# Kernel tuning notes

Measured on AMD Instinct MI355X. Metric: run time of the kernel, lower is better.

## Reference

```python
import jax, jax.numpy as jnp
import numpy as np

D_MODEL = 1024
N_HEADS = 16
D_HEAD = D_MODEL // N_HEADS
SCALE = float(np.sqrt(D_HEAD))


def setup_inputs() -> dict:
    key = jax.random.key(0)
    ks = jax.random.split(key, 9)
    B, S = 2, 2048
    x = jax.random.normal(ks[0], (B, S, D_MODEL), dtype=jnp.float32)
    mask = jnp.tril(jnp.ones((S, S), dtype=jnp.int32))  # causal mask, 0 = masked
    std = 1.0 / np.sqrt(D_MODEL)
    Wq = jax.random.normal(ks[1], (D_MODEL, D_MODEL), dtype=jnp.float32) * std
    bq = jnp.zeros((D_MODEL,), dtype=jnp.float32)
    Wk = jax.random.normal(ks[2], (D_MODEL, D_MODEL), dtype=jnp.float32) * std
    bk = jnp.zeros((D_MODEL,), dtype=jnp.float32)
    Wv = jax.random.normal(ks[3], (D_MODEL, D_MODEL), dtype=jnp.float32) * std
    bv = jnp.zeros((D_MODEL,), dtype=jnp.float32)
    Wo = jax.random.normal(ks[4], (D_MODEL, D_MODEL), dtype=jnp.float32) * std
    bo = jnp.zeros((D_MODEL,), dtype=jnp.float32)
    return {"x": x, "mask": mask, "Wq": Wq, "bq": bq, "Wk": Wk, "bk": bk,
            "Wv": Wv, "bv": bv, "Wo": Wo, "bo": bo}


def reference(x, mask, Wq, bq, Wk, bk, Wv, bv, Wo, bo):
    B, S, _ = x.shape
    # projections (PyTorch Linear: x @ W.T + b; here W stored as [in, out])
    Q = (x @ Wq + bq).reshape(B, S, N_HEADS, D_HEAD).transpose(0, 2, 1, 3)
    K = (x @ Wk + bk).reshape(B, S, N_HEADS, D_HEAD).transpose(0, 2, 1, 3)
    V = (x @ Wv + bv).reshape(B, S, N_HEADS, D_HEAD).transpose(0, 2, 1, 3)
    scores = jnp.einsum('bhqd,bhkd->bhqk', Q, K) / SCALE  # [B,H,S,S]
    scores = jnp.where(mask == 0, -jnp.inf, scores)
    attn = jax.nn.softmax(scores, axis=-1)  # dropout p=0 -> identity
    ctx = jnp.einsum('bhqk,bhkd->bhqd', attn, V)
    ctx = ctx.transpose(0, 2, 1, 3).reshape(B, S, D_MODEL)
    return ctx @ Wo + bo
```

## Files before the change

kernel.cpp:

```cpp
#include <hip/hip_runtime.h>
#include <stdint.h>
#include <math.h>

typedef unsigned short u16;
typedef __attribute__((ext_vector_type(8))) short short8;
typedef __attribute__((ext_vector_type(4))) float f32x4;

#define DEV __device__ __forceinline__

DEV u16 f2b(float f) {
  union { float f; uint32_t u; } v; v.f = f;
  uint32_t r = v.u + 0x7FFFu + ((v.u >> 16) & 1u);
  return (u16)(r >> 16);
}

DEV f32x4 mfma16(short8 a, short8 b, f32x4 c) {
  return __builtin_amdgcn_mfma_f32_16x16x32_bf16(a, b, c, 0, 0, 0);
}

DEV void gload_lds16(const void* g, void* l) {
  __builtin_amdgcn_global_load_lds(
      (const __attribute__((address_space(1))) void*)g,
      (__attribute__((address_space(3))) void*)l, 16, 0, 0);
}

__global__ __launch_bounds__(256) void pack_x_kernel(const float* __restrict__ x,
                                                     u16* __restrict__ xb) {
  int i = blockIdx.x * 256 + threadIdx.x;
  float4 v = reinterpret_cast<const float4*>(x)[i];
  ushort4 o;
  o.x = f2b(v.x); o.y = f2b(v.y); o.z = f2b(v.z); o.w = f2b(v.w);
  reinterpret_cast<ushort4*>(xb)[i] = o;
}

__global__ __launch_bounds__(256) void pack_w4_kernel(
    const float* __restrict__ W0, const float* __restrict__ W1,
    const float* __restrict__ W2, const float* __restrict__ W3,
    u16* __restrict__ T0, u16* __restrict__ T1, u16* __restrict__ T2, u16* __restrict__ T3) {
  const float* W; u16* T;
  switch (blockIdx.z) {
    case 0: W = W0; T = T0; break;
    case 1: W = W1; T = T1; break;
    case 2: W = W2; T = T2; break;
    default: W = W3; T = T3; break;
  }
  __shared__ float t[32][33];
  const int tx = threadIdx.x, ty = threadIdx.y;
  const int n0 = blockIdx.x * 32, k0 = blockIdx.y * 32;
#pragma unroll
  for (int i = 0; i < 32; i += 8)
    t[ty + i][tx] = W[(size_t)(k0 + ty + i) * 1024 + n0 + tx];
  __syncthreads();
#pragma unroll
  for (int i = 0; i < 32; i += 8)
    T[(size_t)(n0 + ty + i) * 1024 + k0 + tx] = f2b(t[tx][ty + i]);
}

template <int MODE>
__global__ __launch_bounds__(256) void gemm_bt_kernel(
    const u16* __restrict__ A, const u16* __restrict__ Bt,
    const float* __restrict__ bias, const float* __restrict__ bias2,
    void* __restrict__ out, int M_, int N_, int K_, float scale) {
  const int tid = threadIdx.x;
  const int w = tid >> 6, l = tid & 63;
  const int g = l >> 4, lr = l & 15;
  const int wr = w >> 1, wc = w & 1;
  const int bm = blockIdx.y, bn = blockIdx.x;

  __shared__ __align__(16) u16 Als[2][128 * 32];
  __shared__ __align__(16) u16 Bls[2][128 * 32];

  f32x4 acc[4][4] = {};

  const int nk = K_ >> 5;
  const int arow = tid >> 2;
  const int acol = (tid & 3) * 8;

  auto stage = [&](int buf, int kt) {
    const int kk = kt * 32 + acol;
#pragma unroll
    for (int i = 0; i < 2; ++i) {
      const u16* asrc = A + (size_t)(bm * 128 + i * 64 + arow) * K_ + kk;
      gload_lds16(asrc, (char*)&Als[buf][0] + i * 4096 + w * 1024);
      const u16* bsrc = Bt + (size_t)(bn * 128 + i * 64 + arow) * K_ + kk;
      gload_lds16(bsrc, (char*)&Bls[buf][0] + i * 4096 + w * 1024);
    }
  };

  stage(0, 0);
  __syncthreads();

  for (int kt = 0; kt < nk; ++kt) {
    const int cur = kt & 1;
    if (kt + 1 < nk) stage(cur ^ 1, kt + 1);
    short8 af[4], bf[4];
#pragma unroll
    for (int i = 0; i < 4; ++i)
      af[i] = *reinterpret_cast<const short8*>(&Als[cur][(wr * 64 + i * 16 + lr) * 32 + g * 8]);
#pragma unroll
    for (int j = 0; j < 4; ++j)
      bf[j] = *reinterpret_cast<const short8*>(&Bls[cur][(wc * 64 + j * 16 + lr) * 32 + g * 8]);
#pragma unroll
    for (int i = 0; i < 4; ++i)
#pragma unroll
      for (int j = 0; j < 4; ++j)
        acc[i][j] = mfma16(af[i], bf[j], acc[i][j]);
    __syncthreads();
  }

#pragma unroll
  for (int i = 0; i < 4; ++i) {
#pragma unroll
    for (int j = 0; j < 4; ++j) {
#pragma unroll
      for (int r = 0; r < 4; ++r) {
        const int row = bm * 128 + wr * 64 + i * 16 + g * 4 + r;
        const int col = bn * 128 + wc * 64 + j * 16 + lr;
        const float v = acc[i][j][r];
        if constexpr (MODE == 0) {
          ((float*)out)[(size_t)row * N_ + col] = v + bias[col];
        } else if constexpr (MODE == 2) {
          const int proj = col >> 10;
          const int c = col & 1023;
          const int b = row >> 11, s = row & 2047;
          const int h = c >> 6, d = c & 63;
          const float bi = proj ? bias2[c] : bias[c];
          const float sc = proj ? 1.0f : scale;
          ((u16*)out)[(size_t)proj * 4194304 +
                      (((size_t)(b * 16 + h)) * 2048 + s) * 64 + d] = f2b((v + bi) * sc);
        } else {
          const int b = col >> 11, s = col & 2047;
          ((u16*)out)[((size_t)(b * 1024 + row)) * 2048 + s] = f2b(v + bias[row]);
        }
      }
    }
  }
}

__global__ __launch_bounds__(256) void attn_kernel(
    const u16* __restrict__ Qg, const u16* __restrict__ Kg,
    const u16* __restrict__ Vt, u16* __restrict__ Og) {
  const int lin = blockIdx.x;
  const int xcd = lin & 7, jj = lin >> 3;
  const int bh = xcd * 4 + (jj >> 4);
  const int pair = jj & 15;
  const int b = bh >> 4, h = bh & 15;
  const int tid = threadIdx.x;
  const int w = tid >> 6, l = tid & 63;
  const int g = l >> 4, lr = l & 15;

  __shared__ __align__(16) u16 Kls[2][64 * 64];
  __shared__ __align__(16) u16 Vls[2][64 * 64];
  __shared__ __align__(16) u16 Pl[4][16 * 88];
  u16* myP = &Pl[w][0];

  const u16* Kbh = Kg + (size_t)bh * 2048 * 64;
  const u16* Vbh = Vt + ((size_t)(b * 1024 + h * 64)) * 2048;

  auto stage = [&](int buf, int kt) {
    const int k0 = kt * 64;
#pragma unroll
    for (int i = 0; i < 2; ++i) {
      const int slot = i * 256 + w * 64 + l;
      const int row = slot >> 3, ch = slot & 7;
      const int cs = ch ^ (row & 7);
      gload_lds16(Kbh + (size_t)(k0 + row) * 64 + cs * 8,
                  (char*)&Kls[buf][0] + (i * 256 + w * 64) * 16);
      gload_lds16(Vbh + (size_t)row * 2048 + k0 + cs * 8,
                  (char*)&Vls[buf][0] + (i * 256 + w * 64) * 16);
    }
  };

  auto rdfrag = [&](const u16* tile, int sub, int hf) -> short8 {
    const int row = sub * 16 + lr;
    const int ch = (hf * 4 + g) ^ (row & 7);
    return *reinterpret_cast<const short8*>(tile + row * 64 + ch * 8);
  };

  for (int t = 0; t < 2; ++t) {
    const int Q = t ? 31 - pair : pair;
    const int q0 = Q * 64 + w * 16;

    const u16* qp = Qg + ((size_t)bh * 2048 + q0 + lr) * 64 + g * 8;
    const short8 qf0 = *reinterpret_cast<const short8*>(qp);
    const short8 qf1 = *reinterpret_cast<const short8*>(qp + 32);

    float lsum[4] = {0.f, 0.f, 0.f, 0.f};
    f32x4 ctx[4] = {};

    stage(0, 0);
    __syncthreads();

    for (int kt = 0; kt <= Q; ++kt) {
      const int cur = kt & 1;
      if (kt < Q) stage(cur ^ 1, kt + 1);
      const u16* Kt = &Kls[cur][0];
      const u16* Vl = &Vls[cur][0];
      const int diag = (kt == Q);
      const int jmax = diag ? (w + 1) : 4;

      f32x4 s[4];
#pragma unroll
      for (int j = 0; j < 4; ++j) {
        if (j < jmax) {
          f32x4 z = {0.f, 0.f, 0.f, 0.f};
          z = mfma16(qf0, rdfrag(Kt, j, 0), z);
          s[j] = mfma16(qf1, rdfrag(Kt, j, 1), z);
          if (diag && j == w) {
#pragma unroll
            for (int r = 0; r < 4; ++r)
              if (lr > g * 4 + r) s[j][r] = -1e30f;
          }
        } else {
          s[j] = (f32x4){-1e30f, -1e30f, -1e30f, -1e30f};
        }
      }

#pragma unroll
      for (int j = 0; j < 4; ++j)
#pragma unroll
        for (int r = 0; r < 4; ++r) {
          const float p = exp2f(s[j][r] - 15.f);
          lsum[r] += p;
          myP[(g * 4 + r) * 88 + j * 16 + lr] = f2b(p);
        }
      const short8 pf0 = *reinterpret_cast<const short8*>(&myP[lr * 88 + g * 8]);
      const short8 pf1 = *reinterpret_cast<const short8*>(&myP[lr * 88 + 32 + g * 8]);
#pragma unroll
      for (int jd = 0; jd < 4; ++jd) {
        ctx[jd] = mfma16(pf0, rdfrag(Vl, jd, 0), ctx[jd]);
        ctx[jd] = mfma16(pf1, rdfrag(Vl, jd, 1), ctx[jd]);
      }
      __syncthreads();
    }

#pragma unroll
    for (int r = 0; r < 4; ++r) {
      float rs = lsum[r];
      rs += __shfl_xor(rs, 1);
      rs += __shfl_xor(rs, 2);
      rs += __shfl_xor(rs, 4);
      rs += __shfl_xor(rs, 8);
      lsum[r] = 1.f / rs;
    }
#pragma unroll
    for (int jd = 0; jd < 4; ++jd)
#pragma unroll
      for (int r = 0; r < 4; ++r) {
        const int q = q0 + g * 4 + r;
        Og[((size_t)(b * 2048 + q)) * 1024 + h * 64 + jd * 16 + lr] =
            f2b(ctx[jd][r] * lsum[r]);
      }
  }
}

extern "C" void kernel_launch(void* const* d_in, const int* in_sizes, int n_in,
                              void* d_out, int out_size, void* d_ws, size_t ws_size,
                              hipStream_t stream) {
  const float* x  = (const float*)d_in[0];
  const float* Wq = (const float*)d_in[2];
  const float* bq = (const float*)d_in[3];
  const float* Wk = (const float*)d_in[4];
  const float* bk = (const float*)d_in[5];
  const float* Wv = (const float*)d_in[6];
  const float* bv = (const float*)d_in[7];
  const float* Wo = (const float*)d_in[8];
  const float* bo = (const float*)d_in[9];

  char* ws = (char*)d_ws;
  const size_t MB = (size_t)1 << 20;
  u16* xb  = (u16*)(ws + 0 * MB);
  u16* wqt = (u16*)(ws + 8 * MB);
  u16* wkt = (u16*)(ws + 10 * MB);
  u16* wvt = (u16*)(ws + 12 * MB);
  u16* wot = (u16*)(ws + 14 * MB);
  u16* Qg  = (u16*)(ws + 16 * MB);
  u16* Kg  = (u16*)(ws + 24 * MB);
  u16* Vt  = (u16*)(ws + 32 * MB);
  u16* Og  = (u16*)(ws + 40 * MB);

  const float QSCALE = 0.125f * 1.44269504f;

  pack_x_kernel<<<4096, 256, 0, stream>>>(x, xb);
  pack_w4_kernel<<<dim3(32, 32, 4), dim3(32, 8), 0, stream>>>(
      Wq, Wk, Wv, Wo, wqt, wkt, wvt, wot);
  gemm_bt_kernel<2><<<dim3(16, 32), 256, 0, stream>>>(
      xb, wqt, bq, bk, Qg, 4096, 2048, 1024, QSCALE);
  gemm_bt_kernel<3><<<dim3(32, 8), 256, 0, stream>>>(
      wvt, xb, bv, nullptr, Vt, 1024, 4096, 1024, 1.0f);
  attn_kernel<<<512, 256, 0, stream>>>(Qg, Kg, Vt, Og);
  gemm_bt_kernel<0><<<dim3(8, 32), 256, 0, stream>>>(
      Og, wot, bo, nullptr, d_out, 4096, 1024, 1024, 1.0f);
}
```

Measured before the change: 139.0 us.

## Merge QK and V projections into one launch and rework attention scheduling

Combines the QK and V projection GEMMs into a single kernel of 768 blocks, so there is one launch and the two halves run concurrently. The attention kernel now gives each block one query tile, largest first, in a grid of 1024 blocks, instead of pairing tiles per block. It computes S transposed (K as the A operand), packs probabilities with v_cvt_pk_bf16_f32, drops the -15 offset in exp2, and raises wave priority around the MFMA sections. The output GEMM is specialized with constant sizes. Removing the exponent offset raises the risk of overflow for large scores.

Measured after the change: 143.8 us. +3.4%, slower.

```diff
diff --git a/kernel.cpp b/kernel.cpp
--- a/kernel.cpp
+++ b/kernel.cpp
@@ -4,6 +4,7 @@
 
 typedef unsigned short u16;
 typedef __attribute__((ext_vector_type(8))) short short8;
+typedef __attribute__((ext_vector_type(2))) unsigned u32x2;
 typedef __attribute__((ext_vector_type(4))) float f32x4;
 
 #define DEV __device__ __forceinline__
@@ -12,6 +13,12 @@
   union { float f; uint32_t u; } v; v.f = f;
   uint32_t r = v.u + 0x7FFFu + ((v.u >> 16) & 1u);
   return (u16)(r >> 16);
+}
+
+DEV unsigned cvtpk(float a, float b) {
+  unsigned r;
+  asm("v_cvt_pk_bf16_f32 %0, %1, %2" : "=v"(r) : "v"(a), "v"(b));
+  return r;
 }
 
 DEV f32x4 mfma16(short8 a, short8 b, f32x4 c) {
@@ -56,23 +63,30 @@
     T[(size_t)(n0 + ty + i) * 1024 + k0 + tx] = f2b(t[tx][ty + i]);
 }
 
-template <int MODE>
-__global__ __launch_bounds__(256) void gemm_bt_kernel(
-    const u16* __restrict__ A, const u16* __restrict__ Bt,
-    const float* __restrict__ bias, const float* __restrict__ bias2,
-    void* __restrict__ out, int M_, int N_, int K_, float scale) {
+__global__ __launch_bounds__(256) void proj_kernel(
+    const u16* __restrict__ xb, const u16* __restrict__ wqkt,
+    const float* __restrict__ bq, const float* __restrict__ bk,
+    const u16* __restrict__ wvt, const float* __restrict__ bv,
+    u16* __restrict__ Qg, u16* __restrict__ Vt, float qscale) {
+  const int blk = blockIdx.x;
+  const u16 *A, *Bt;
+  int bm, bn;
+  bool isV;
+  if (blk < 512) {
+    isV = false; bn = blk & 15; bm = blk >> 4; A = xb; Bt = wqkt;
+  } else {
+    isV = true; const int idx = blk - 512; bn = idx & 31; bm = idx >> 5; A = wvt; Bt = xb;
+  }
+
   const int tid = threadIdx.x;
   const int w = tid >> 6, l = tid & 63;
   const int g = l >> 4, lr = l & 15;
   const int wr = w >> 1, wc = w & 1;
-  const int bm = blockIdx.y, bn = blockIdx.x;
 
   __shared__ __align__(16) u16 Als[2][128 * 32];
   __shared__ __align__(16) u16 Bls[2][128 * 32];
 
   f32x4 acc[4][4] = {};
-
-  const int nk = K_ >> 5;
   const int arow = tid >> 2;
   const int acol = (tid & 3) * 8;
 
@@ -80,19 +94,19 @@
     const int kk = kt * 32 + acol;
 #pragma unroll
     for (int i = 0; i < 2; ++i) {
-      const u16* asrc = A + (size_t)(bm * 128 + i * 64 + arow) * K_ + kk;
-      gload_lds16(asrc, (char*)&Als[buf][0] + i * 4096 + w * 1024);
-      const u16* bsrc = Bt + (size_t)(bn * 128 + i * 64 + arow) * K_ + kk;
-      gload_lds16(bsrc, (char*)&Bls[buf][0] + i * 4096 + w * 1024);
+      gload_lds16(A + (size_t)(bm * 128 + i * 64 + arow) * 1024 + kk,
+                  (char*)&Als[buf][0] + i * 4096 + w * 1024);
+      gload_lds16(Bt + (size_t)(bn * 128 + i * 64 + arow) * 1024 + kk,
+                  (char*)&Bls[buf][0] + i * 4096 + w * 1024);
     }
   };
 
   stage(0, 0);
   __syncthreads();
 
-  for (int kt = 0; kt < nk; ++kt) {
+  for (int kt = 0; kt < 32; ++kt) {
     const int cur = kt & 1;
-    if (kt + 1 < nk) stage(cur ^ 1, kt + 1);
+    if (kt + 1 < 32) stage(cur ^ 1, kt + 1);
     short8 af[4], bf[4];
 #pragma unroll
     for (int i = 0; i < 4; ++i)
@@ -117,20 +131,18 @@
         const int row = bm * 128 + wr * 64 + i * 16 + g * 4 + r;
         const int col = bn * 128 + wc * 64 + j * 16 + lr;
         const float v = acc[i][j][r];
-        if constexpr (MODE == 0) {
-          ((float*)out)[(size_t)row * N_ + col] = v + bias[col];
-        } else if constexpr (MODE == 2) {
+        if (!isV) {
           const int proj = col >> 10;
           const int c = col & 1023;
           const int b = row >> 11, s = row & 2047;
           const int h = c >> 6, d = c & 63;
-          const float bi = proj ? bias2[c] : bias[c];
-          const float sc = proj ? 1.0f : scale;
-          ((u16*)out)[(size_t)proj * 4194304 +
-                      (((size_t)(b * 16 + h)) * 2048 + s) * 64 + d] = f2b((v + bi) * sc);
+          const float bi = proj ? bk[c] : bq[c];
+          const float sc = proj ? 1.0f : qscale;
+          Qg[(size_t)proj * 4194304 +
+             (((size_t)(b * 16 + h)) * 2048 + s) * 64 + d] = f2b((v + bi) * sc);
         } else {
           const int b = col >> 11, s = col & 2047;
-          ((u16*)out)[((size_t)(b * 1024 + row)) * 2048 + s] = f2b(v + bias[row]);
+          Vt[((size_t)(b * 1024 + row)) * 2048 + s] = f2b(v + bv[row]);
         }
       }
     }
@@ -141,9 +153,9 @@
     const u16* __restrict__ Qg, const u16* __restrict__ Kg,
     const u16* __restrict__ Vt, u16* __restrict__ Og) {
   const int lin = blockIdx.x;
-  const int xcd = lin & 7, jj = lin >> 3;
-  const int bh = xcd * 4 + (jj >> 4);
-  const int pair = jj & 15;
+  const int xcd = lin & 7, idx = lin >> 3;
+  const int bh = xcd * 4 + (idx >> 5);
+  const int qt = 31 - (idx & 31);
   const int b = bh >> 4, h = bh & 15;
   const int tid = threadIdx.x;
   const int w = tid >> 6, l = tid & 63;
@@ -151,9 +163,9 @@
 
   __shared__ __align__(16) u16 Kls[2][64 * 64];
   __shared__ __align__(16) u16 Vls[2][64 * 64];
-  __shared__ __align__(16) u16 Pl[4][16 * 88];
+  __shared__ __align__(16) u16 Pl[4][16 * 80];
+
   u16* myP = &Pl[w][0];
-
   const u16* Kbh = Kg + (size_t)bh * 2048 * 64;
   const u16* Vbh = Vt + ((size_t)(b * 1024 + h * 64)) * 2048;
 
@@ -177,81 +189,140 @@
     return *reinterpret_cast<const short8*>(tile + row * 64 + ch * 8);
   };
 
-  for (int t = 0; t < 2; ++t) {
-    const int Q = t ? 31 - pair : pair;
-    const int q0 = Q * 64 + w * 16;
-
-    const u16* qp = Qg + ((size_t)bh * 2048 + q0 + lr) * 64 + g * 8;
-    const short8 qf0 = *reinterpret_cast<const short8*>(qp);
-    const short8 qf1 = *reinterpret_cast<const short8*>(qp + 32);
-
-    float lsum[4] = {0.f, 0.f, 0.f, 0.f};
-    f32x4 ctx[4] = {};
-
-    stage(0, 0);
+  const int q0 = qt * 64 + w * 16;
+  const u16* qp = Qg + ((size_t)bh * 2048 + q0 + lr) * 64 + g * 8;
+  const short8 qf0 = *reinterpret_cast<const short8*>(qp);
+  const short8 qf1 = *reinterpret_cast<const short8*>(qp + 32);
+
+  float lsum = 0.f;
+  f32x4 ctx[4] = {};
+
+  stage(0, 0);
+  __syncthreads();
+
+  for (int kt = 0; kt <= qt; ++kt) {
+    const int cur = kt & 1;
+    if (kt < qt) stage(cur ^ 1, kt + 1);
+    const u16* Kt = &Kls[cur][0];
+    const u16* Vl = &Vls[cur][0];
+    const int diag = (kt == qt);
+    const int jmax = diag ? (w + 1) : 4;
+
+    f32x4 s[4];
+    __builtin_amdgcn_s_setprio(1);
+#pragma unroll
+    for (int j = 0; j < 4; ++j) {
+      if (j < jmax) {
+        f32x4 z = {0.f, 0.f, 0.f, 0.f};
+        z = mfma16(rdfrag(Kt, j, 0), qf0, z);
+        s[j] = mfma16(rdfrag(Kt, j, 1), qf1, z);
+        if (diag && j == w) {
+#pragma unroll
+          for (int r = 0; r < 4; ++r)
+            if (g * 4 + r > lr) s[j][r] = -1e30f;
+        }
+      } else {
+        s[j] = (f32x4){-1e30f, -1e30f, -1e30f, -1e30f};
+      }
+    }
+    __builtin_amdgcn_s_setprio(0);
+
+#pragma unroll
+    for (int j = 0; j < 4; ++j) {
+      const float p0 = exp2f(s[j][0]), p1 = exp2f(s[j][1]);
+      const float p2 = exp2f(s[j][2]), p3 = exp2f(s[j][3]);
+      lsum += (p0 + p1) + (p2 + p3);
+      u32x2 pk;
+      pk.x = cvtpk(p0, p1);
+      pk.y = cvtpk(p2, p3);
+      *reinterpret_cast<u32x2*>(&myP[lr * 80 + j * 16 + g * 4]) = pk;
+    }
+    const short8 pa0 = *reinterpret_cast<const short8*>(&myP[lr * 80 + g * 8]);
+    const short8 pa1 = *reinterpret_cast<const short8*>(&myP[lr * 80 + 32 + g * 8]);
+
+    __builtin_amdgcn_s_setprio(1);
+#pragma unroll
+    for (int jd = 0; jd < 4; ++jd) {
+      ctx[jd] = mfma16(pa0, rdfrag(Vl, jd, 0), ctx[jd]);
+      ctx[jd] = mfma16(pa1, rdfrag(Vl, jd, 1), ctx[jd]);
+    }
+    __builtin_amdgcn_s_setprio(0);
     __syncthreads();
-
-    for (int kt = 0; kt <= Q; ++kt) {
-      const int cur = kt & 1;
-      if (kt < Q) stage(cur ^ 1, kt + 1);
-      const u16* Kt = &Kls[cur][0];
-      const u16* Vl = &Vls[cur][0];
-      const int diag = (kt == Q);
-      const int jmax = diag ? (w + 1) : 4;
-
-      f32x4 s[4];
-#pragma unroll
-      for (int j = 0; j < 4; ++j) {
-        if (j < jmax) {
-          f32x4 z = {0.f, 0.f, 0.f, 0.f};
-          z = mfma16(qf0, rdfrag(Kt, j, 0), z);
-          s[j] = mfma16(qf1, rdfrag(Kt, j, 1), z);
-          if (diag && j == w) {
-#pragma unroll
-            for (int r = 0; r < 4; ++r)
-              if (lr > g * 4 + r) s[j][r] = -1e30f;
-          }
-        } else {
-          s[j] = (f32x4){-1e30f, -1e30f, -1e30f, -1e30f};
-        }
+  }
+
+  lsum += __shfl_xor(lsum, 16);
+  lsum += __shfl_xor(lsum, 32);
+  float inv[4];
+#pragma unroll
+  for (int r = 0; r < 4; ++r) inv[r] = 1.f / __shfl(lsum, g * 4 + r);
+#pragma unroll
+  for (int jd = 0; jd < 4; ++jd)
+#pragma unroll
+    for (int r = 0; r < 4; ++r) {
+      const int q = q0 + g * 4 + r;
+      Og[((size_t)(b * 2048 + q)) * 1024 + h * 64 + jd * 16 + lr] =
+          f2b(ctx[jd][r] * inv[r]);
+    }
+}
+
+__global__ __launch_bounds__(256) void gemm_o_kernel(
+    const u16* __restrict__ A, const u16* __restrict__ Bt,
+    const float* __restrict__ bias, float* __restrict__ out) {
+  const int tid = threadIdx.x;
+  const int w = tid >> 6, l = tid & 63;
+  const int g = l >> 4, lr = l & 15;
+  const int wr = w >> 1, wc = w & 1;
+  const int bm = blockIdx.y, bn = blockIdx.x;
+
+  __shared__ __align__(16) u16 Als[2][128 * 32];
+  __shared__ __align__(16) u16 Bls[2][128 * 32];
+
+  f32x4 acc[4][4] = {};
+  const int arow = tid >> 2;
+  const int acol = (tid & 3) * 8;
+
+  auto stage = [&](int buf, int kt) {
+    const int kk = kt * 32 + acol;
+#pragma unroll
+    for (int i = 0; i < 2; ++i) {
+      gload_lds16(A + (size_t)(bm * 128 + i * 64 + arow) * 1024 + kk,
+                  (char*)&Als[buf][0] + i * 4096 + w * 1024);
+      gload_lds16(Bt + (size_t)(bn * 128 + i * 64 + arow) * 1024 + kk,
+                  (char*)&Bls[buf][0] + i * 4096 + w * 1024);
+    }
+  };
+
+  stage(0, 0);
+  __syncthreads();
+
+  for (int kt = 0; kt < 32; ++kt) {
+    const int cur = kt & 1;
+    if (kt + 1 < 32) stage(cur ^ 1, kt + 1);
+    short8 af[4], bf[4];
+#pragma unroll
+    for (int i = 0; i < 4; ++i)
+      af[i] = *reinterpret_cast<const short8*>(&Als[cur][(wr * 64 + i * 16 + lr) * 32 + g * 8]);
+#pragma unroll
+    for (int j = 0; j < 4; ++j)
+      bf[j] = *reinterpret_cast<const short8*>(&Bls[cur][(wc * 64 + j * 16 + lr) * 32 + g * 8]);
+#pragma unroll
+    for (int i = 0; i < 4; ++i)
+#pragma unroll
+      for (int j = 0; j < 4; ++j)
+        acc[i][j] = mfma16(af[i], bf[j], acc[i][j]);
+    __syncthreads();
+  }
+
+#pragma unroll
+  for (int i = 0; i < 4; ++i)
+#pragma unroll
+    for (int j = 0; j < 4; ++j)
+#pragma unroll
+      for (int r = 0; r < 4; ++r) {
+        const int row = bm * 128 + wr * 64 + i * 16 + g * 4 + r;
+        const int col = bn * 128 + wc * 64 + j * 16 + lr;
+        out[(size_t)row * 1024 + col] = acc[i][j][r] + bias[col];
       }
-
-#pragma unroll
-      for (int j = 0; j < 4; ++j)
-#pragma unroll
-        for (int r = 0; r < 4; ++r) {
-          const float p = exp2f(s[j][r] - 15.f);
-          lsum[r] += p;
-          myP[(g * 4 + r) * 88 + j * 16 + lr] = f2b(p);
-        }
-      const short8 pf0 = *reinterpret_cast<const short8*>(&myP[lr * 88 + g * 8]);
-      const short8 pf1 = *reinterpret_cast<const short8*>(&myP[lr * 88 + 32 + g * 8]);
-#pragma unroll
-      for (int jd = 0; jd < 4; ++jd) {
-        ctx[jd] = mfma16(pf0, rdfrag(Vl, jd, 0), ctx[jd]);
-        ctx[jd] = mfma16(pf1, rdfrag(Vl, jd, 1), ctx[jd]);
-      }
-      __syncthreads();
-    }
-
-#pragma unroll
-    for (int r = 0; r < 4; ++r) {
-      float rs = lsum[r];
-      rs += __shfl_xor(rs, 1);
-      rs += __shfl_xor(rs, 2);
-      rs += __shfl_xor(rs, 4);
-      rs += __shfl_xor(rs, 8);
-      lsum[r] = 1.f / rs;
-    }
-#pragma unroll
-    for (int jd = 0; jd < 4; ++jd)
-#pragma unroll
-      for (int r = 0; r < 4; ++r) {
-        const int q = q0 + g * 4 + r;
-        Og[((size_t)(b * 2048 + q)) * 1024 + h * 64 + jd * 16 + lr] =
-            f2b(ctx[jd][r] * lsum[r]);
-      }
-  }
 }
 
 extern "C" void kernel_launch(void* const* d_in, const int* in_sizes, int n_in,
@@ -284,11 +355,7 @@
   pack_x_kernel<<<4096, 256, 0, stream>>>(x, xb);
   pack_w4_kernel<<<dim3(32, 32, 4), dim3(32, 8), 0, stream>>>(
       Wq, Wk, Wv, Wo, wqt, wkt, wvt, wot);
-  gemm_bt_kernel<2><<<dim3(16, 32), 256, 0, stream>>>(
-      xb, wqt, bq, bk, Qg, 4096, 2048, 1024, QSCALE);
-  gemm_bt_kernel<3><<<dim3(32, 8), 256, 0, stream>>>(
-      wvt, xb, bv, nullptr, Vt, 1024, 4096, 1024, 1.0f);
-  attn_kernel<<<512, 256, 0, stream>>>(Qg, Kg, Vt, Og);
-  gemm_bt_kernel<0><<<dim3(8, 32), 256, 0, stream>>>(
-      Og, wot, bo, nullptr, d_out, 4096, 1024, 1024, 1.0f);
-}
+  proj_kernel<<<768, 256, 0, stream>>>(xb, wqt, bq, bk, wvt, bv, Qg, Vt, QSCALE);
+  attn_kernel<<<1024, 256, 0, stream>>>(Qg, Kg, Vt, Og);
+  gemm_o_kernel<<<dim3(8, 32), 256, 0, stream>>>(Og, wot, bo, (float*)d_out);
+}
```

## Merge pack kernels, use 128x64 GEMM tiles, one q-tile per attention block

Applied to the files above, without the earlier changes.

The two packing kernels become one launch that indexes on a flat block id. The V and output projections move to a 128x64-tile GEMM that launches twice as many blocks, and the QK projection gets a specialized kernel with hardcoded K. Attention now handles one query tile per block, 1024 blocks with heavy tiles scheduled first, instead of pairing tiles within a block. It also raises wave priority around the MFMA sections. Together these aim to cut launch overhead and improve CU occupancy and load balance, at the cost of more blocks and less reuse per tile.

After: 146.8 us. +5.6%, slower.

```diff
diff --git a/kernel.cpp b/kernel.cpp
--- a/kernel.cpp
+++ b/kernel.cpp
@@ -24,29 +24,32 @@
       (__attribute__((address_space(3))) void*)l, 16, 0, 0);
 }
 
-__global__ __launch_bounds__(256) void pack_x_kernel(const float* __restrict__ x,
-                                                     u16* __restrict__ xb) {
-  int i = blockIdx.x * 256 + threadIdx.x;
-  float4 v = reinterpret_cast<const float4*>(x)[i];
-  ushort4 o;
-  o.x = f2b(v.x); o.y = f2b(v.y); o.z = f2b(v.z); o.w = f2b(v.w);
-  reinterpret_cast<ushort4*>(xb)[i] = o;
-}
-
-__global__ __launch_bounds__(256) void pack_w4_kernel(
+__global__ __launch_bounds__(256) void pack_all_kernel(
+    const float* __restrict__ x, u16* __restrict__ xb,
     const float* __restrict__ W0, const float* __restrict__ W1,
     const float* __restrict__ W2, const float* __restrict__ W3,
-    u16* __restrict__ T0, u16* __restrict__ T1, u16* __restrict__ T2, u16* __restrict__ T3) {
+    u16* __restrict__ T0, u16* __restrict__ T1, u16* __restrict__ T2,
+    u16* __restrict__ T3) {
+  const int blk = blockIdx.x;
+  const int tid = threadIdx.x;
+  if (blk >= 4096) {
+    const int i = (blk - 4096) * 256 + tid;
+    float4 v = reinterpret_cast<const float4*>(x)[i];
+    ushort4 o;
+    o.x = f2b(v.x); o.y = f2b(v.y); o.z = f2b(v.z); o.w = f2b(v.w);
+    reinterpret_cast<ushort4*>(xb)[i] = o;
+    return;
+  }
   const float* W; u16* T;
-  switch (blockIdx.z) {
+  switch (blk >> 10) {
     case 0: W = W0; T = T0; break;
     case 1: W = W1; T = T1; break;
     case 2: W = W2; T = T2; break;
     default: W = W3; T = T3; break;
   }
   __shared__ float t[32][33];
-  const int tx = threadIdx.x, ty = threadIdx.y;
-  const int n0 = blockIdx.x * 32, k0 = blockIdx.y * 32;
+  const int tx = tid & 31, ty = tid >> 5;
+  const int n0 = (blk & 31) * 32, k0 = ((blk >> 5) & 31) * 32;
 #pragma unroll
   for (int i = 0; i < 32; i += 8)
     t[ty + i][tx] = W[(size_t)(k0 + ty + i) * 1024 + n0 + tx];
@@ -56,11 +59,10 @@
     T[(size_t)(n0 + ty + i) * 1024 + k0 + tx] = f2b(t[tx][ty + i]);
 }
 
-template <int MODE>
-__global__ __launch_bounds__(256) void gemm_bt_kernel(
+__global__ __launch_bounds__(256) void gemm_qk_kernel(
     const u16* __restrict__ A, const u16* __restrict__ Bt,
     const float* __restrict__ bias, const float* __restrict__ bias2,
-    void* __restrict__ out, int M_, int N_, int K_, float scale) {
+    u16* __restrict__ out, float scale) {
   const int tid = threadIdx.x;
   const int w = tid >> 6, l = tid & 63;
   const int g = l >> 4, lr = l & 15;
@@ -71,8 +73,6 @@
   __shared__ __align__(16) u16 Bls[2][128 * 32];
 
   f32x4 acc[4][4] = {};
-
-  const int nk = K_ >> 5;
   const int arow = tid >> 2;
   const int acol = (tid & 3) * 8;
 
@@ -80,19 +80,19 @@
     const int kk = kt * 32 + acol;
 #pragma unroll
     for (int i = 0; i < 2; ++i) {
-      const u16* asrc = A + (size_t)(bm * 128 + i * 64 + arow) * K_ + kk;
-      gload_lds16(asrc, (char*)&Als[buf][0] + i * 4096 + w * 1024);
-      const u16* bsrc = Bt + (size_t)(bn * 128 + i * 64 + arow) * K_ + kk;
-      gload_lds16(bsrc, (char*)&Bls[buf][0] + i * 4096 + w * 1024);
+      gload_lds16(A + (size_t)(bm * 128 + i * 64 + arow) * 1024 + kk,
+                  (char*)&Als[buf][0] + i * 4096 + w * 1024);
+      gload_lds16(Bt + (size_t)(bn * 128 + i * 64 + arow) * 1024 + kk,
+                  (char*)&Bls[buf][0] + i * 4096 + w * 1024);
     }
   };
 
   stage(0, 0);
   __syncthreads();
 
-  for (int kt = 0; kt < nk; ++kt) {
+  for (int kt = 0; kt < 32; ++kt) {
     const int cur = kt & 1;
-    if (kt + 1 < nk) stage(cur ^ 1, kt + 1);
+    if (kt + 1 < 32) stage(cur ^ 1, kt + 1);
     short8 af[4], bf[4];
 #pragma unroll
     for (int i = 0; i < 4; ++i)
@@ -109,41 +109,98 @@
   }
 
 #pragma unroll
-  for (int i = 0; i < 4; ++i) {
-#pragma unroll
-    for (int j = 0; j < 4; ++j) {
+  for (int i = 0; i < 4; ++i)
+#pragma unroll
+    for (int j = 0; j < 4; ++j)
 #pragma unroll
       for (int r = 0; r < 4; ++r) {
         const int row = bm * 128 + wr * 64 + i * 16 + g * 4 + r;
         const int col = bn * 128 + wc * 64 + j * 16 + lr;
         const float v = acc[i][j][r];
+        const int proj = col >> 10;
+        const int c = col & 1023;
+        const int b = row >> 11, s = row & 2047;
+        const int h = c >> 6, d = c & 63;
+        const float bi = proj ? bias2[c] : bias[c];
+        const float sc = proj ? 1.0f : scale;
+        out[(size_t)proj * 4194304 +
+            (((size_t)(b * 16 + h)) * 2048 + s) * 64 + d] = f2b((v + bi) * sc);
+      }
+}
+
+template <int MODE>
+__global__ __launch_bounds__(256) void gemm64_kernel(
+    const u16* __restrict__ A, const u16* __restrict__ Bt,
+    const float* __restrict__ bias, void* __restrict__ out) {
+  const int tid = threadIdx.x;
+  const int w = tid >> 6, l = tid & 63;
+  const int g = l >> 4, lr = l & 15;
+  const int wr = w >> 1, wc = w & 1;
+  const int bm = blockIdx.y, bn = blockIdx.x;
+
+  __shared__ __align__(16) u16 Als[2][128 * 32];
+  __shared__ __align__(16) u16 Bls[2][64 * 32];
+
+  f32x4 acc[4][2] = {};
+
+  auto stage = [&](int buf, int kt) {
+    const int kk0 = kt * 32;
+#pragma unroll
+    for (int i = 0; i < 2; ++i) {
+      const int s = i * 256 + tid;
+      gload_lds16(A + (size_t)(bm * 128 + (s >> 2)) * 1024 + kk0 + (s & 3) * 8,
+                  (char*)&Als[buf][0] + (i * 256) * 16 + (tid) * 16);
+    }
+    gload_lds16(Bt + (size_t)(bn * 64 + (tid >> 2)) * 1024 + kk0 + (tid & 3) * 8,
+                (char*)&Bls[buf][0] + tid * 16);
+  };
+
+  stage(0, 0);
+  __syncthreads();
+
+  for (int kt = 0; kt < 32; ++kt) {
+    const int cur = kt & 1;
+    if (kt + 1 < 32) stage(cur ^ 1, kt + 1);
+    short8 af[4], bf[2];
+#pragma unroll
+    for (int i = 0; i < 4; ++i)
+      af[i] = *reinterpret_cast<const short8*>(&Als[cur][(wr * 64 + i * 16 + lr) * 32 + g * 8]);
+#pragma unroll
+    for (int j = 0; j < 2; ++j)
+      bf[j] = *reinterpret_cast<const short8*>(&Bls[cur][(wc * 32 + j * 16 + lr) * 32 + g * 8]);
+#pragma unroll
+    for (int i = 0; i < 4; ++i)
+#pragma unroll
+      for (int j = 0; j < 2; ++j)
+        acc[i][j] = mfma16(af[i], bf[j], acc[i][j]);
+    __syncthreads();
+  }
+
+#pragma unroll
+  for (int i = 0; i < 4; ++i)
+#pragma unroll
+    for (int j = 0; j < 2; ++j)
+#pragma unroll
+      for (int r = 0; r < 4; ++r) {
+        const int row = bm * 128 + wr * 64 + i * 16 + g * 4 + r;
+        const int col = bn * 64 + wc * 32 + j * 16 + lr;
+        const float v = acc[i][j][r];
         if constexpr (MODE == 0) {
-          ((float*)out)[(size_t)row * N_ + col] = v + bias[col];
-        } else if constexpr (MODE == 2) {
-          const int proj = col >> 10;
-          const int c = col & 1023;
-          const int b = row >> 11, s = row & 2047;
-          const int h = c >> 6, d = c & 63;
-          const float bi = proj ? bias2[c] : bias[c];
-          const float sc = proj ? 1.0f : scale;
-          ((u16*)out)[(size_t)proj * 4194304 +
-                      (((size_t)(b * 16 + h)) * 2048 + s) * 64 + d] = f2b((v + bi) * sc);
+          ((float*)out)[(size_t)row * 1024 + col] = v + bias[col];
         } else {
           const int b = col >> 11, s = col & 2047;
           ((u16*)out)[((size_t)(b * 1024 + row)) * 2048 + s] = f2b(v + bias[row]);
         }
       }
-    }
-  }
 }
 
 __global__ __launch_bounds__(256) void attn_kernel(
     const u16* __restrict__ Qg, const u16* __restrict__ Kg,
     const u16* __restrict__ Vt, u16* __restrict__ Og) {
   const int lin = blockIdx.x;
-  const int xcd = lin & 7, jj = lin >> 3;
-  const int bh = xcd * 4 + (jj >> 4);
-  const int pair = jj & 15;
+  const int xcd = lin & 7, idx = lin >> 3;
+  const int bh = xcd * 4 + (idx >> 5);
+  const int qt = 31 - (idx & 31);
   const int b = bh >> 4, h = bh & 15;
   const int tid = threadIdx.x;
   const int w = tid >> 6, l = tid & 63;
@@ -152,8 +209,8 @@
   __shared__ __align__(16) u16 Kls[2][64 * 64];
   __shared__ __align__(16) u16 Vls[2][64 * 64];
   __shared__ __align__(16) u16 Pl[4][16 * 88];
+
   u16* myP = &Pl[w][0];
-
   const u16* Kbh = Kg + (size_t)bh * 2048 * 64;
   const u16* Vbh = Vt + ((size_t)(b * 1024 + h * 64)) * 2048;
 
@@ -177,81 +234,82 @@
     return *reinterpret_cast<const short8*>(tile + row * 64 + ch * 8);
   };
 
-  for (int t = 0; t < 2; ++t) {
-    const int Q = t ? 31 - pair : pair;
-    const int q0 = Q * 64 + w * 16;
-
-    const u16* qp = Qg + ((size_t)bh * 2048 + q0 + lr) * 64 + g * 8;
-    const short8 qf0 = *reinterpret_cast<const short8*>(qp);
-    const short8 qf1 = *reinterpret_cast<const short8*>(qp + 32);
-
-    float lsum[4] = {0.f, 0.f, 0.f, 0.f};
-    f32x4 ctx[4] = {};
-
-    stage(0, 0);
+  const int q0 = qt * 64 + w * 16;
+  const u16* qp = Qg + ((size_t)bh * 2048 + q0 + lr) * 64 + g * 8;
+  const short8 qf0 = *reinterpret_cast<const short8*>(qp);
+  const short8 qf1 = *reinterpret_cast<const short8*>(qp + 32);
+
+  float lsum[4] = {0.f, 0.f, 0.f, 0.f};
+  f32x4 ctx[4] = {};
+
+  stage(0, 0);
+  __syncthreads();
+
+  for (int kt = 0; kt <= qt; ++kt) {
+    const int cur = kt & 1;
+    if (kt < qt) stage(cur ^ 1, kt + 1);
+    const u16* Kt = &Kls[cur][0];
+    const u16* Vl = &Vls[cur][0];
+    const int diag = (kt == qt);
+    const int jmax = diag ? (w + 1) : 4;
+
+    f32x4 s[4];
+    __builtin_amdgcn_s_setprio(1);
+#pragma unroll
+    for (int j = 0; j < 4; ++j) {
+      if (j < jmax) {
+        f32x4 z = {0.f, 0.f, 0.f, 0.f};
+        z = mfma16(qf0, rdfrag(Kt, j, 0), z);
+        s[j] = mfma16(qf1, rdfrag(Kt, j, 1), z);
+        if (diag && j == w) {
+#pragma unroll
+          for (int r = 0; r < 4; ++r)
+            if (lr > g * 4 + r) s[j][r] = -1e30f;
+        }
+      } else {
+        s[j] = (f32x4){-1e30f, -1e30f, -1e30f, -1e30f};
+      }
+    }
+    __builtin_amdgcn_s_setprio(0);
+
+#pragma unroll
+    for (int j = 0; j < 4; ++j)
+#pragma unroll
+      for (int r = 0; r < 4; ++r) {
+        const float p = exp2f(s[j][r] - 15.f);
+        lsum[r] += p;
+        myP[(g * 4 + r) * 88 + j * 16 + lr] = f2b(p);
+      }
+    const short8 pf0 = *reinterpret_cast<const short8*>(&myP[lr * 88 + g * 8]);
+    const short8 pf1 = *reinterpret_cast<const short8*>(&myP[lr * 88 + 32 + g * 8]);
+
+    __builtin_amdgcn_s_setprio(1);
+#pragma unroll
+    for (int jd = 0; jd < 4; ++jd) {
+      ctx[jd] = mfma16(pf0, rdfrag(Vl, jd, 0), ctx[jd]);
+      ctx[jd] = mfma16(pf1, rdfrag(Vl, jd, 1), ctx[jd]);
+    }
+    __builtin_amdgcn_s_setprio(0);
     __syncthreads();
-
-    for (int kt = 0; kt <= Q; ++kt) {
-      const int cur = kt & 1;
-      if (kt < Q) stage(cur ^ 1, kt + 1);
-      const u16* Kt = &Kls[cur][0];
-      const u16* Vl = &Vls[cur][0];
-      const int diag = (kt == Q);
-      const int jmax = diag ? (w + 1) : 4;
-
-      f32x4 s[4];
-#pragma unroll
-      for (int j = 0; j < 4; ++j) {
-        if (j < jmax) {
-          f32x4 z = {0.f, 0.f, 0.f, 0.f};
-          z = mfma16(qf0, rdfrag(Kt, j, 0), z);
-          s[j] = mfma16(qf1, rdfrag(Kt, j, 1), z);
-          if (diag && j == w) {
-#pragma unroll
-            for (int r = 0; r < 4; ++r)
-              if (lr > g * 4 + r) s[j][r] = -1e30f;
-          }
-        } else {
-          s[j] = (f32x4){-1e30f, -1e30f, -1e30f, -1e30f};
-        }
-      }
-
-#pragma unroll
-      for (int j = 0; j < 4; ++j)
-#pragma unroll
-        for (int r = 0; r < 4; ++r) {
-          const float p = exp2f(s[j][r] - 15.f);
-          lsum[r] += p;
-          myP[(g * 4 + r) * 88 + j * 16 + lr] = f2b(p);
-        }
-      const short8 pf0 = *reinterpret_cast<const short8*>(&myP[lr * 88 + g * 8]);
-      const short8 pf1 = *reinterpret_cast<const short8*>(&myP[lr * 88 + 32 + g * 8]);
-#pragma unroll
-      for (int jd = 0; jd < 4; ++jd) {
-        ctx[jd] = mfma16(pf0, rdfrag(Vl, jd, 0), ctx[jd]);
-        ctx[jd] = mfma16(pf1, rdfrag(Vl, jd, 1), ctx[jd]);
-      }
-      __syncthreads();
-    }
-
+  }
+
+#pragma unroll
+  for (int r = 0; r < 4; ++r) {
+    float rs = lsum[r];
+    rs += __shfl_xor(rs, 1);
+    rs += __shfl_xor(rs, 2);
+    rs += __shfl_xor(rs, 4);
+    rs += __shfl_xor(rs, 8);
+    lsum[r] = 1.f / rs;
+  }
+#pragma unroll
+  for (int jd = 0; jd < 4; ++jd)
 #pragma unroll
     for (int r = 0; r < 4; ++r) {
-      float rs = lsum[r];
-      rs += __shfl_xor(rs, 1);
-      rs += __shfl_xor(rs, 2);
-      rs += __shfl_xor(rs, 4);
-      rs += __shfl_xor(rs, 8);
-      lsum[r] = 1.f / rs;
-    }
-#pragma unroll
-    for (int jd = 0; jd < 4; ++jd)
-#pragma unroll
-      for (int r = 0; r < 4; ++r) {
-        const int q = q0 + g * 4 + r;
-        Og[((size_t)(b * 2048 + q)) * 1024 + h * 64 + jd * 16 + lr] =
-            f2b(ctx[jd][r] * lsum[r]);
-      }
-  }
+      const int q = q0 + g * 4 + r;
+      Og[((size_t)(b * 2048 + q)) * 1024 + h * 64 + jd * 16 + lr] =
+          f2b(ctx[jd][r] * lsum[r]);
+    }
 }
 
 extern "C" void kernel_launch(void* const* d_in, const int* in_sizes, int n_in,
@@ -281,14 +339,10 @@
 
   const float QSCALE = 0.125f * 1.44269504f;
 
-  pack_x_kernel<<<4096, 256, 0, stream>>>(x, xb);
-  pack_w4_kernel<<<dim3(32, 32, 4), dim3(32, 8), 0, stream>>>(
-      Wq, Wk, Wv, Wo, wqt, wkt, wvt, wot);
-  gemm_bt_kernel<2><<<dim3(16, 32), 256, 0, stream>>>(
-      xb, wqt, bq, bk, Qg, 4096, 2048, 1024, QSCALE);
-  gemm_bt_kernel<3><<<dim3(32, 8), 256, 0, stream>>>(
-      wvt, xb, bv, nullptr, Vt, 1024, 4096, 1024, 1.0f);
-  attn_kernel<<<512, 256, 0, stream>>>(Qg, Kg, Vt, Og);
-  gemm_bt_kernel<0><<<dim3(8, 32), 256, 0, stream>>>(
-      Og, wot, bo, nullptr, d_out, 4096, 1024, 1024, 1.0f);
-}
+  pack_all_kernel<<<8192, 256, 0, stream>>>(x, xb, Wq, Wk, Wv, Wo,
+                                            wqt, wkt, wvt, wot);
+  gemm_qk_kernel<<<dim3(16, 32), 256, 0, stream>>>(xb, wqt, bq, bk, Qg, QSCALE);
+  gemm64_kernel<3><<<dim3(64, 8), 256, 0, stream>>>(wvt, xb, bv, Vt);
+  attn_kernel<<<1024, 256, 0, stream>>>(Qg, Kg, Vt, Og);
+  gemm64_kernel<0><<<dim3(16, 32), 256, 0, stream>>>(Og, wot, bo, d_out);
+}
```
